# Kernel optimization log

Measured on AMD Instinct MI355X. Metric: run time of the kernel, lower is better.

The kernel has to match this reference:

```python
import jax, jax.numpy as jnp
import numpy as np
from jax import lax

LOOKBACK = 48
HORIZON = 12
INPUT_DIM = 8
OUTPUT_DIM = 1
HIDDEN = 128
NUM_LAYERS = 2
BG_IDX = 0
BATCH = 8192


def _lstm_cell(x, h, c, W_ih, W_hh, b_ih, b_hh):
    # x:[B,Din] h,c:[B,H]; PyTorch gate order i,f,g,o
    g = x @ W_ih.T + h @ W_hh.T + b_ih + b_hh
    i, f, gg, o = jnp.split(g, 4, axis=-1)
    c_new = jax.nn.sigmoid(f) * c + jax.nn.sigmoid(i) * jnp.tanh(gg)
    h_new = jax.nn.sigmoid(o) * jnp.tanh(c_new)
    return h_new, c_new


def setup_inputs() -> dict:
    key = jax.random.key(0)
    ks = jax.random.split(key, 16)
    k_scale = 1.0 / np.sqrt(HIDDEN)
    u = lambda k, shp: jax.random.uniform(k, shp, jnp.float32, -k_scale, k_scale)
    inp = {
        "inputs": jax.random.normal(ks[0], (BATCH, LOOKBACK + HORIZON, INPUT_DIM), jnp.float32),
        "W_ih_0": u(ks[1], (4 * HIDDEN, INPUT_DIM)),
        "W_hh_0": u(ks[2], (4 * HIDDEN, HIDDEN)),
        "b_ih_0": u(ks[3], (4 * HIDDEN,)),
        "b_hh_0": u(ks[4], (4 * HIDDEN,)),
        "W_ih_1": u(ks[5], (4 * HIDDEN, HIDDEN)),
        "W_hh_1": u(ks[6], (4 * HIDDEN, HIDDEN)),
        "b_ih_1": u(ks[7], (4 * HIDDEN,)),
        "b_hh_1": u(ks[8], (4 * HIDDEN,)),
        "W_fc": u(ks[9], (OUTPUT_DIM, HIDDEN)),
        "b_fc": u(ks[10], (OUTPUT_DIM,)),
    }
    return inp


def _forward(inputs, params, W_fc, b_fc):
    B = inputs.shape[0]
    # ---- encode lookback window, layer by layer (time-major scan) ----
    xs = jnp.swapaxes(inputs[:, :LOOKBACK, :], 0, 1)  # [T,B,D]
    finals_h, finals_c = [], []
    for (Wi, Wh, bi, bh) in params:
        h0 = jnp.zeros((B, HIDDEN), inputs.dtype)
        c0 = jnp.zeros((B, HIDDEN), inputs.dtype)
        def cell(carry, x, Wi=Wi, Wh=Wh, bi=bi, bh=bh):
            h, c = carry
            h, c = _lstm_cell(x, h, c, Wi, Wh, bi, bh)
            return (h, c), h
        (hT, cT), xs = lax.scan(cell, (h0, c0), xs)
        finals_h.append(hT)
        finals_c.append(cT)
    hs0 = jnp.stack(finals_h)  # [L,B,H]
    cs0 = jnp.stack(finals_c)

    dec_xs = jnp.swapaxes(inputs[:, LOOKBACK:, :], 0, 1)  # [Th,B,D]
    ts = jnp.arange(HORIZON)

    def step(carry, inp):
        hs, cs, last_bg = carry
        x, t = inp
        bg = jnp.where(t > 0, last_bg, x[:, BG_IDX])
        x = x.at[:, BG_IDX].set(bg)
        new_hs, new_cs = [], []
        cur = x
        for l, (Wi, Wh, bi, bh) in enumerate(params):
            h, c = _lstm_cell(cur, hs[l], cs[l], Wi, Wh, bi, bh)
            new_hs.append(h)
            new_cs.append(c)
            cur = h
        pred = cur @ W_fc.T + b_fc  # [B,O]
        return (jnp.stack(new_hs), jnp.stack(new_cs), pred[:, 0]), pred

    init = (hs0, cs0, jnp.zeros((B,), inputs.dtype))
    _, preds = lax.scan(step, init, (dec_xs, ts))  # [Th,B,O]
    return jnp.swapaxes(preds, 0, 1)  # [B,Th,O]


def reference(inputs, W_ih_0, W_hh_0, b_ih_0, b_hh_0, W_ih_1, W_hh_1, b_ih_1, b_hh_1, W_fc, b_fc):
    params = [(W_ih_0, W_hh_0, b_ih_0, b_hh_0), (W_ih_1, W_hh_1, b_ih_1, b_hh_1)]
    return _forward(inputs, params, W_fc, b_fc)
```

## Files before the change

### kernel.cpp

```cpp
#include <hip/hip_runtime.h>

#define LOOKBACK 48
#define HORIZON  12
#define TTOT     60
#define INPUT_DIM 8
#define HIDDEN   128
#define GATES    512
#define BATCH    8192
#define TILE_B   32
#define NTHREADS 512
#define NSLICES  8
#define L0_KS    5
#define L1_KS    8
#define FRAGS_PER_KS 4
#define FRAG_SHORTS 512
#define KSTRIDE  (FRAGS_PER_KS * FRAG_SHORTS)
#define SLICE_FRAGS ((L0_KS + L1_KS) * FRAGS_PER_KS)
#define W_HALFS  (NSLICES * SLICE_FRAGS * FRAG_SHORTS)

#define ROWP 33
#define A0_CHUNKS 20
#define A1_CHUNKS 16
#define A0_BUF (A0_CHUNKS * ROWP * 8)
#define A1_BUF (A1_CHUNKS * ROWP * 8)
#define A0_HALFS (2 * A0_BUF)
#define A1_HALFS (2 * A1_BUF)

typedef __attribute__((ext_vector_type(8))) _Float16 half8;
typedef __attribute__((ext_vector_type(4))) float f32x4;

__device__ __forceinline__ float frcp(float x) { return __builtin_amdgcn_rcpf(x); }
__device__ __forceinline__ float sigm(float x) {
    return frcp(1.0f + __expf(-x));
}
__device__ __forceinline__ float tanh_fast(float x) {
    float ax = fabsf(x);
    float e  = __expf(-2.0f * ax);
    float t  = (1.0f - e) * frcp(1.0f + e);
    return copysignf(t, x);
}

#define BARRIER() __asm__ volatile("s_waitcnt lgkmcnt(0)\ns_barrier" ::: "memory")

__global__ void setup_kernel(const float* __restrict__ Wih0, const float* __restrict__ Whh0,
                             const float* __restrict__ bi0,  const float* __restrict__ bh0,
                             const float* __restrict__ Wih1, const float* __restrict__ Whh1,
                             const float* __restrict__ bi1,  const float* __restrict__ bh1,
                             _Float16* __restrict__ wfrag, float* __restrict__ bias) {
    int idx = blockIdx.x * blockDim.x + threadIdx.x;
    if (idx < W_HALFS) {
        int e = idx & 511, frag = idx >> 9;
        int lane = e >> 3, j = e & 7;
        int t = frag & 3;
        int rest = frag >> 2;
        int lks = rest % (L0_KS + L1_KS), s = rest / (L0_KS + L1_KS);
        int l = (lks < L0_KS) ? 0 : 1;
        int ks = l ? (lks - L0_KS) : lks;
        int k = ks * 32 + ((lane >> 4) << 3) + j;
        int uu = s * 16 + (lane & 15);
        int row = t * HIDDEN + uu;
        float v = 0.0f;
        if (l == 0) {
            if (k < INPUT_DIM) v = Wih0[row * INPUT_DIM + k];
            else if (k < INPUT_DIM + HIDDEN) v = Whh0[row * HIDDEN + (k - INPUT_DIM)];
        } else {
            if (k < HIDDEN) v = Wih1[row * HIDDEN + k];
            else v = Whh1[row * HIDDEN + (k - HIDDEN)];
        }
        wfrag[idx] = (_Float16)v;
    } else if (idx < W_HALFS + 2 * GATES) {
        int g = idx - W_HALFS;
        bias[g] = (g < GATES) ? (bi0[g] + bh0[g]) : (bi1[g - GATES] + bh1[g - GATES]);
    }
}

__global__ __launch_bounds__(NTHREADS, 2)
void lstm_kernel(const float* __restrict__ input,
                 const _Float16* __restrict__ wfrag,
                 const float* __restrict__ bias01,
                 const float* __restrict__ W_fc,
                 const float* __restrict__ b_fc,
                 float* __restrict__ out) {
    __shared__ _Float16 A0[A0_HALFS];
    __shared__ _Float16 A1[A1_HALFS];
    __shared__ float wfcs[HIDDEN];

    const int tid  = threadIdx.x;
    const int lane = tid & 63;
    const int s    = tid >> 6;
    const int col  = lane & 15;
    const int quad = lane >> 4;
    const int u    = s * 16 + col;
    const int batch0 = blockIdx.x * TILE_B;

    uintptr_t wp64 = (uintptr_t)(wfrag + s * (SLICE_FRAGS * FRAG_SHORTS));
    wp64 = ((uintptr_t)__builtin_amdgcn_readfirstlane((unsigned)(wp64 >> 32)) << 32)
         | __builtin_amdgcn_readfirstlane((unsigned)wp64);
    const _Float16* wbase = (const _Float16*)wp64;

    for (int i = tid; i < A0_HALFS; i += NTHREADS) A0[i] = (_Float16)0.f;
    for (int i = tid; i < A1_HALFS; i += NTHREADS) A1[i] = (_Float16)0.f;
    if (tid < HIDDEN) wfcs[tid] = W_fc[tid];
    const float bfc = b_fc[0];

    float bv0[4], bv1[4];
#pragma unroll
    for (int tt = 0; tt < 4; ++tt) {
        bv0[tt] = bias01[tt * HIDDEN + u];
        bv1[tt] = bias01[GATES + tt * HIDDEN + u];
    }

    float c0[2][4] = {}, c1[2][4] = {};

    float xv = 0.0f;
    if (tid < TILE_B * INPUT_DIM)
        xv = input[(size_t)(batch0 + (tid >> 3)) * (TTOT * INPUT_DIM) + (tid & 7)];
    BARRIER();
    if (tid < TILE_B * INPUT_DIM)
        A0[(tid >> 3) * 8 + (tid & 7)] = (_Float16)xv;

    half8 bq[3][4];
    half8 ah[2][2];

#define LOADB(p, sl) {                                                          \
    _Pragma("unroll") for (int tt = 0; tt < 4; ++tt)                            \
        bq[sl][tt] = *(const half8*)(wbase + (p) * KSTRIDE                      \
                                     + tt * FRAG_SHORTS + lane * 8); }
#define LOADA(H, off, chunk, buf) { int base_ = (off) + ((chunk) * ROWP + col) * 8; \
    ah[buf][0] = *(const half8*)(H + base_);                                    \
    ah[buf][1] = *(const half8*)(H + base_ + 16 * 8); }
#define COMP(ACC, ab, sl)                                                       \
    _Pragma("unroll") for (int tt = 0; tt < 4; ++tt)                            \
    _Pragma("unroll") for (int mt = 0; mt < 2; ++mt)                            \
        ACC[mt][tt] = __builtin_amdgcn_mfma_f32_16x16x32_f16(                   \
            ah[ab][mt], bq[sl][tt], ACC[mt][tt], 0, 0, 0);

    LOADB(0, 0) LOADB(1, 1) LOADB(2, 2)
    BARRIER();

#pragma unroll 1
    for (int t = 0; t < TTOT; ++t) {
        const int rb = t & 1, wb = rb ^ 1;
        const int a0r = rb * A0_BUF, a0w = wb * A0_BUF;
        const int a1r = rb * A1_BUF, a1w = wb * A1_BUF;

        if (tid < TILE_B * INPUT_DIM && t + 1 < TTOT)
            xv = input[(size_t)(batch0 + (tid >> 3)) * (TTOT * INPUT_DIM)
                       + (t + 1) * INPUT_DIM + (tid & 7)];

        f32x4 acc[2][4];
#pragma unroll
        for (int tt = 0; tt < 4; ++tt) {
            f32x4 b = {bv0[tt], bv0[tt], bv0[tt], bv0[tt]};
            acc[0][tt] = b; acc[1][tt] = b;
        }
        LOADA(A0, a0r, quad, 0)
        LOADA(A0, a0r, 4 + quad, 1)  COMP(acc, 0, 0) LOADB(3, 0)
        LOADA(A0, a0r, 8 + quad, 0)  COMP(acc, 1, 1) LOADB(4, 1)
        LOADA(A0, a0r, 12 + quad, 1) COMP(acc, 0, 2) LOADB(5, 2)
        LOADA(A0, a0r, 16 + quad, 0) COMP(acc, 1, 0) LOADB(6, 0)
                                     COMP(acc, 0, 1) LOADB(7, 1)

#pragma unroll
        for (int mt = 0; mt < 2; ++mt) {
#pragma unroll
            for (int r = 0; r < 4; ++r) {
                float ig = sigm(acc[mt][0][r]);
                float fg = sigm(acc[mt][1][r]);
                float gg = tanh_fast(acc[mt][2][r]);
                float og = sigm(acc[mt][3][r]);
                float cn = fg * c0[mt][r] + ig * gg;
                c0[mt][r] = cn;
                float h = og * tanh_fast(cn);
                int row = mt * 16 + quad * 4 + r;
                A0[a0w + ((1 + (u >> 3)) * ROWP + row) * 8 + (u & 7)] = (_Float16)h;
            }
        }
        if (tid < TILE_B * INPUT_DIM && t + 1 < TTOT) {
            int r = tid >> 3, k = tid & 7;
            if (!(t + 1 > LOOKBACK && k == 0))
                A0[a0w + r * 8 + k] = (_Float16)xv;
        }
        BARRIER();

#pragma unroll
        for (int tt = 0; tt < 4; ++tt) {
            f32x4 b = {bv1[tt], bv1[tt], bv1[tt], bv1[tt]};
            acc[0][tt] = b; acc[1][tt] = b;
        }
        LOADA(A0, a0w, 1 + quad, 0)
        LOADA(A0, a0w, 5 + quad, 1)   COMP(acc, 0, 2) LOADB(8, 2)
        LOADA(A0, a0w, 9 + quad, 0)   COMP(acc, 1, 0) LOADB(9, 0)
        LOADA(A0, a0w, 13 + quad, 1)  COMP(acc, 0, 1) LOADB(10, 1)
        LOADA(A1, a1r, quad, 0)       COMP(acc, 1, 2) LOADB(11, 2)
        LOADA(A1, a1r, 4 + quad, 1)   COMP(acc, 0, 0) LOADB(12, 0)
        LOADA(A1, a1r, 8 + quad, 0)   COMP(acc, 1, 1) LOADB(1, 1)
        LOADA(A1, a1r, 12 + quad, 1)  COMP(acc, 0, 2) LOADB(2, 2)
                                      COMP(acc, 1, 0) LOADB(0, 0)

#pragma unroll
        for (int mt = 0; mt < 2; ++mt) {
#pragma unroll
            for (int r = 0; r < 4; ++r) {
                float ig = sigm(acc[mt][0][r]);
                float fg = sigm(acc[mt][1][r]);
                float gg = tanh_fast(acc[mt][2][r]);
                float og = sigm(acc[mt][3][r]);
                float cn = fg * c1[mt][r] + ig * gg;
                c1[mt][r] = cn;
                float h = og * tanh_fast(cn);
                int row = mt * 16 + quad * 4 + r;
                A1[a1w + ((u >> 3) * ROWP + row) * 8 + (u & 7)] = (_Float16)h;
            }
        }

        if (t >= LOOKBACK) {
            BARRIER();
            int r = tid >> 4, sub = tid & 15;
            float p = 0.0f;
#pragma unroll
            for (int i = 0; i < HIDDEN / 16; ++i) {
                int uu = sub + i * 16;
                p += (float)A1[a1w + ((uu >> 3) * ROWP + r) * 8 + (uu & 7)] * wfcs[uu];
            }
#pragma unroll
            for (int off = 8; off; off >>= 1) p += __shfl_down(p, off, 16);
            if (sub == 0) {
                float pr = p + bfc;
                out[(size_t)(batch0 + r) * HORIZON + (t - LOOKBACK)] = pr;
                if (t + 1 < TTOT)
                    A0[a0w + r * 8] = (_Float16)pr;
            }
            BARRIER();
        }
    }
#undef LOADB
#undef LOADA
#undef COMP
}

extern "C" void kernel_launch(void* const* d_in, const int* in_sizes, int n_in,
                              void* d_out, int out_size, void* d_ws, size_t ws_size,
                              hipStream_t stream) {
    const float* input = (const float*)d_in[0];
    const float* Wih0  = (const float*)d_in[1];
    const float* Whh0  = (const float*)d_in[2];
    const float* bi0   = (const float*)d_in[3];
    const float* bh0   = (const float*)d_in[4];
    const float* Wih1  = (const float*)d_in[5];
    const float* Whh1  = (const float*)d_in[6];
    const float* bi1   = (const float*)d_in[7];
    const float* bh1   = (const float*)d_in[8];
    const float* W_fc  = (const float*)d_in[9];
    const float* b_fc  = (const float*)d_in[10];

    _Float16* wfrag = (_Float16*)d_ws;
    float* bias = (float*)((char*)d_ws + (size_t)W_HALFS * sizeof(_Float16));

    int total = W_HALFS + 2 * GATES;
    setup_kernel<<<(total + 255) / 256, 256, 0, stream>>>(
        Wih0, Whh0, bi0, bh0, Wih1, Whh1, bi1, bh1, wfrag, bias);

    lstm_kernel<<<BATCH / TILE_B, NTHREADS, 0, stream>>>(
        input, wfrag, bias, W_fc, b_fc, (float*)d_out);
}
```

Before: 374.5 us.

## Unroll time loop by two and prefetch next step's layer-0 A fragments

The time loop is unrolled by two through a STEP macro, so the double-buffer offsets become compile-time constants. During the lookback phase, the first layer-0 A fragments for the next step are loaded at the end of the current step, so they overlap the tail work instead of stalling the next step's first MFMAs. Decode steps still reload at the start because the fed-back prediction changes the input. tanh is rewritten as 2*sigmoid(2x)-1, which needs fewer instructions but loses some precision near zero and raises register pressure.

Result: no change. 370.9 us (-1.0%).

```diff
diff --git a/kernel.cpp b/kernel.cpp
--- a/kernel.cpp
+++ b/kernel.cpp
@@ -12,10 +12,11 @@
 #define NSLICES  8
 #define L0_KS    5
 #define L1_KS    8
+#define NPOS     (L0_KS + L1_KS)
 #define FRAGS_PER_KS 4
 #define FRAG_SHORTS 512
 #define KSTRIDE  (FRAGS_PER_KS * FRAG_SHORTS)
-#define SLICE_FRAGS ((L0_KS + L1_KS) * FRAGS_PER_KS)
+#define SLICE_FRAGS (NPOS * FRAGS_PER_KS)
 #define W_HALFS  (NSLICES * SLICE_FRAGS * FRAG_SHORTS)
 
 #define ROWP 33
@@ -34,10 +35,7 @@
     return frcp(1.0f + __expf(-x));
 }
 __device__ __forceinline__ float tanh_fast(float x) {
-    float ax = fabsf(x);
-    float e  = __expf(-2.0f * ax);
-    float t  = (1.0f - e) * frcp(1.0f + e);
-    return copysignf(t, x);
+    return __builtin_fmaf(2.0f, frcp(1.0f + __expf(-2.0f * x)), -1.0f);
 }
 
 #define BARRIER() __asm__ volatile("s_waitcnt lgkmcnt(0)\ns_barrier" ::: "memory")
@@ -53,7 +51,7 @@
         int lane = e >> 3, j = e & 7;
         int t = frag & 3;
         int rest = frag >> 2;
-        int lks = rest % (L0_KS + L1_KS), s = rest / (L0_KS + L1_KS);
+        int lks = rest % NPOS, s = rest / NPOS;
         int l = (lks < L0_KS) ? 0 : 1;
         int ks = l ? (lks - L0_KS) : lks;
         int k = ks * 32 + ((lane >> 4) << 3) + j;
@@ -112,12 +110,14 @@
 
     float c0[2][4] = {}, c1[2][4] = {};
 
-    float xv = 0.0f;
-    if (tid < TILE_B * INPUT_DIM)
-        xv = input[(size_t)(batch0 + (tid >> 3)) * (TTOT * INPUT_DIM) + (tid & 7)];
-    BARRIER();
-    if (tid < TILE_B * INPUT_DIM)
-        A0[(tid >> 3) * 8 + (tid & 7)] = (_Float16)xv;
+    {
+        float x0 = 0.0f;
+        if (tid < TILE_B * INPUT_DIM)
+            x0 = input[(size_t)(batch0 + (tid >> 3)) * (TTOT * INPUT_DIM) + (tid & 7)];
+        BARRIER();
+        if (tid < TILE_B * INPUT_DIM)
+            A0[(tid >> 3) * 8 + (tid & 7)] = (_Float16)x0;
+    }
 
     half8 bq[3][4];
     half8 ah[2][2];
@@ -129,7 +129,7 @@
 #define LOADA(H, off, chunk, buf) { int base_ = (off) + ((chunk) * ROWP + col) * 8; \
     ah[buf][0] = *(const half8*)(H + base_);                                    \
     ah[buf][1] = *(const half8*)(H + base_ + 16 * 8); }
-#define COMP(ACC, ab, sl)                                                       \
+#define COMPQ(ACC, ab, sl)                                                      \
     _Pragma("unroll") for (int tt = 0; tt < 4; ++tt)                            \
     _Pragma("unroll") for (int mt = 0; mt < 2; ++mt)                            \
         ACC[mt][tt] = __builtin_amdgcn_mfma_f32_16x16x32_f16(                   \
@@ -137,106 +137,117 @@
 
     LOADB(0, 0) LOADB(1, 1) LOADB(2, 2)
     BARRIER();
+    LOADA(A0, 0, quad, 0)
+    LOADA(A0, 0, 4 + quad, 1)
+
+#define STEP(TC, RB) {                                                          \
+    const int a0r = (RB) * A0_BUF, a0w = ((RB) ^ 1) * A0_BUF;                   \
+    const int a1r = (RB) * A1_BUF, a1w = ((RB) ^ 1) * A1_BUF;                   \
+    float xv = 0.0f;                                                            \
+    if (tid < TILE_B * INPUT_DIM && (TC) + 1 < TTOT)                            \
+        xv = input[(size_t)(batch0 + (tid >> 3)) * (TTOT * INPUT_DIM)           \
+                   + ((TC) + 1) * INPUT_DIM + (tid & 7)];                       \
+                     \
+    if ((TC) > LOOKBACK) {                                                      \
+        LOADA(A0, a0r, quad, 0)                                                 \
+        LOADA(A0, a0r, 4 + quad, 1)                                             \
+    }                                                                           \
+                         \
+    f32x4 acc[2][4];                                                            \
+    _Pragma("unroll") for (int tt = 0; tt < 4; ++tt) {                          \
+        f32x4 b = {bv0[tt], bv0[tt], bv0[tt], bv0[tt]};                         \
+        acc[0][tt] = b; acc[1][tt] = b;                                         \
+    }                                                                           \
+    COMPQ(acc, 0, 0) LOADB(3, 0) LOADA(A0, a0r, 8 + quad, 0)                    \
+    COMPQ(acc, 1, 1) LOADB(4, 1) LOADA(A0, a0r, 12 + quad, 1)                   \
+    COMPQ(acc, 0, 2) LOADB(5, 2) LOADA(A0, a0r, 16 + quad, 0)                   \
+    COMPQ(acc, 1, 0) LOADB(6, 0)                                                \
+    COMPQ(acc, 0, 1) LOADB(7, 1)                                                \
+                                  \
+    _Pragma("unroll") for (int mt = 0; mt < 2; ++mt) {                          \
+        _Pragma("unroll") for (int r = 0; r < 4; ++r) {                         \
+            float ig = sigm(acc[mt][0][r]);                                     \
+            float fg = sigm(acc[mt][1][r]);                                     \
+            float gg = tanh_fast(acc[mt][2][r]);                                \
+            float og = sigm(acc[mt][3][r]);                                     \
+            float cn = fg * c0[mt][r] + ig * gg;                                \
+            c0[mt][r] = cn;                                                     \
+            float h = og * tanh_fast(cn);                                       \
+            int row = mt * 16 + quad * 4 + r;                                   \
+            A0[a0w + ((1 + (u >> 3)) * ROWP + row) * 8 + (u & 7)] = (_Float16)h;\
+        }                                                                       \
+    }                                                                           \
+              \
+    if (tid < TILE_B * INPUT_DIM && (TC) + 1 < TTOT) {                          \
+        int r = tid >> 3, k = tid & 7;                                          \
+        if (!((TC) + 1 > LOOKBACK && k == 0))                                   \
+            A0[a0w + r * 8 + k] = (_Float16)xv;                                 \
+    }                                                                           \
+    BARRIER();                                    \
+       \
+    _Pragma("unroll") for (int tt = 0; tt < 4; ++tt) {                          \
+        f32x4 b = {bv1[tt], bv1[tt], bv1[tt], bv1[tt]};                         \
+        acc[0][tt] = b; acc[1][tt] = b;                                         \
+    }                                                                           \
+    LOADA(A0, a0w, 1 + quad, 0)                                                 \
+    LOADA(A0, a0w, 5 + quad, 1)   COMPQ(acc, 0, 2) LOADB(8, 2)                  \
+    LOADA(A0, a0w, 9 + quad, 0)   COMPQ(acc, 1, 0) LOADB(9, 0)                  \
+    LOADA(A0, a0w, 13 + quad, 1)  COMPQ(acc, 0, 1) LOADB(10, 1)                 \
+    LOADA(A1, a1r, quad, 0)       COMPQ(acc, 1, 2) LOADB(11, 2)                 \
+    LOADA(A1, a1r, 4 + quad, 1)   COMPQ(acc, 0, 0) LOADB(12, 0)                 \
+    LOADA(A1, a1r, 8 + quad, 0)   COMPQ(acc, 1, 1) LOADB(1, 1)                  \
+    LOADA(A1, a1r, 12 + quad, 1)  COMPQ(acc, 0, 2) LOADB(2, 2)                  \
+                                  COMPQ(acc, 1, 0) LOADB(0, 0)                  \
+                                               \
+    _Pragma("unroll") for (int mt = 0; mt < 2; ++mt) {                          \
+        _Pragma("unroll") for (int r = 0; r < 4; ++r) {                         \
+            float ig = sigm(acc[mt][0][r]);                                     \
+            float fg = sigm(acc[mt][1][r]);                                     \
+            float gg = tanh_fast(acc[mt][2][r]);                                \
+            float og = sigm(acc[mt][3][r]);                                     \
+            float cn = fg * c1[mt][r] + ig * gg;                                \
+            c1[mt][r] = cn;                                                     \
+            float h = og * tanh_fast(cn);                                       \
+            int row = mt * 16 + quad * 4 + r;                                   \
+            A1[a1w + ((u >> 3) * ROWP + row) * 8 + (u & 7)] = (_Float16)h;      \
+        }                                                                       \
+    }                                                                           \
+       \
+    if ((TC) < LOOKBACK) {                                                      \
+        LOADA(A0, a0w, quad, 0)                                                 \
+        LOADA(A0, a0w, 4 + quad, 1)                                             \
+    }                                                                           \
+                                     \
+    if ((TC) >= LOOKBACK) {                                                     \
+        BARRIER();                                       \
+        int r = tid >> 4, sub = tid & 15;                                       \
+        float p = 0.0f;                                                         \
+        _Pragma("unroll") for (int i = 0; i < HIDDEN / 16; ++i) {               \
+            int uu = sub + i * 16;                                              \
+            p += (float)A1[a1w + ((uu >> 3) * ROWP + r) * 8 + (uu & 7)]         \
+                 * wfcs[uu];                                                    \
+        }                                                                       \
+        _Pragma("unroll") for (int off = 8; off; off >>= 1)                     \
+            p += __shfl_down(p, off, 16);                                       \
+        if (sub == 0) {                                                         \
+            float pr = p + bfc;                                                 \
+            out[(size_t)(batch0 + r) * HORIZON + ((TC) - LOOKBACK)] = pr;       \
+            if ((TC) + 1 < TTOT)                                                \
+                A0[a0w + r * 8] = (_Float16)pr;                                 \
+        }                                                                       \
+        BARRIER();                                     \
+    }                                                                           \
+}
 
 #pragma unroll 1
-    for (int t = 0; t < TTOT; ++t) {
-        const int rb = t & 1, wb = rb ^ 1;
-        const int a0r = rb * A0_BUF, a0w = wb * A0_BUF;
-        const int a1r = rb * A1_BUF, a1w = wb * A1_BUF;
-
-        if (tid < TILE_B * INPUT_DIM && t + 1 < TTOT)
-            xv = input[(size_t)(batch0 + (tid >> 3)) * (TTOT * INPUT_DIM)
-                       + (t + 1) * INPUT_DIM + (tid & 7)];
-
-        f32x4 acc[2][4];
-#pragma unroll
-        for (int tt = 0; tt < 4; ++tt) {
-            f32x4 b = {bv0[tt], bv0[tt], bv0[tt], bv0[tt]};
-            acc[0][tt] = b; acc[1][tt] = b;
-        }
-        LOADA(A0, a0r, quad, 0)
-        LOADA(A0, a0r, 4 + quad, 1)  COMP(acc, 0, 0) LOADB(3, 0)
-        LOADA(A0, a0r, 8 + quad, 0)  COMP(acc, 1, 1) LOADB(4, 1)
-        LOADA(A0, a0r, 12 + quad, 1) COMP(acc, 0, 2) LOADB(5, 2)
-        LOADA(A0, a0r, 16 + quad, 0) COMP(acc, 1, 0) LOADB(6, 0)
-                                     COMP(acc, 0, 1) LOADB(7, 1)
-
-#pragma unroll
-        for (int mt = 0; mt < 2; ++mt) {
-#pragma unroll
-            for (int r = 0; r < 4; ++r) {
-                float ig = sigm(acc[mt][0][r]);
-                float fg = sigm(acc[mt][1][r]);
-                float gg = tanh_fast(acc[mt][2][r]);
-                float og = sigm(acc[mt][3][r]);
-                float cn = fg * c0[mt][r] + ig * gg;
-                c0[mt][r] = cn;
-                float h = og * tanh_fast(cn);
-                int row = mt * 16 + quad * 4 + r;
-                A0[a0w + ((1 + (u >> 3)) * ROWP + row) * 8 + (u & 7)] = (_Float16)h;
-            }
-        }
-        if (tid < TILE_B * INPUT_DIM && t + 1 < TTOT) {
-            int r = tid >> 3, k = tid & 7;
-            if (!(t + 1 > LOOKBACK && k == 0))
-                A0[a0w + r * 8 + k] = (_Float16)xv;
-        }
-        BARRIER();
-
-#pragma unroll
-        for (int tt = 0; tt < 4; ++tt) {
-            f32x4 b = {bv1[tt], bv1[tt], bv1[tt], bv1[tt]};
-            acc[0][tt] = b; acc[1][tt] = b;
-        }
-        LOADA(A0, a0w, 1 + quad, 0)
-        LOADA(A0, a0w, 5 + quad, 1)   COMP(acc, 0, 2) LOADB(8, 2)
-        LOADA(A0, a0w, 9 + quad, 0)   COMP(acc, 1, 0) LOADB(9, 0)
-        LOADA(A0, a0w, 13 + quad, 1)  COMP(acc, 0, 1) LOADB(10, 1)
-        LOADA(A1, a1r, quad, 0)       COMP(acc, 1, 2) LOADB(11, 2)
-        LOADA(A1, a1r, 4 + quad, 1)   COMP(acc, 0, 0) LOADB(12, 0)
-        LOADA(A1, a1r, 8 + quad, 0)   COMP(acc, 1, 1) LOADB(1, 1)
-        LOADA(A1, a1r, 12 + quad, 1)  COMP(acc, 0, 2) LOADB(2, 2)
-                                      COMP(acc, 1, 0) LOADB(0, 0)
-
-#pragma unroll
-        for (int mt = 0; mt < 2; ++mt) {
-#pragma unroll
-            for (int r = 0; r < 4; ++r) {
-                float ig = sigm(acc[mt][0][r]);
-                float fg = sigm(acc[mt][1][r]);
-                float gg = tanh_fast(acc[mt][2][r]);
-                float og = sigm(acc[mt][3][r]);
-                float cn = fg * c1[mt][r] + ig * gg;
-                c1[mt][r] = cn;
-                float h = og * tanh_fast(cn);
-                int row = mt * 16 + quad * 4 + r;
-                A1[a1w + ((u >> 3) * ROWP + row) * 8 + (u & 7)] = (_Float16)h;
-            }
-        }
-
-        if (t >= LOOKBACK) {
-            BARRIER();
-            int r = tid >> 4, sub = tid & 15;
-            float p = 0.0f;
-#pragma unroll
-            for (int i = 0; i < HIDDEN / 16; ++i) {
-                int uu = sub + i * 16;
-                p += (float)A1[a1w + ((uu >> 3) * ROWP + r) * 8 + (uu & 7)] * wfcs[uu];
-            }
-#pragma unroll
-            for (int off = 8; off; off >>= 1) p += __shfl_down(p, off, 16);
-            if (sub == 0) {
-                float pr = p + bfc;
-                out[(size_t)(batch0 + r) * HORIZON + (t - LOOKBACK)] = pr;
-                if (t + 1 < TTOT)
-                    A0[a0w + r * 8] = (_Float16)pr;
-            }
-            BARRIER();
-        }
-    }
+    for (int t = 0; t < TTOT; t += 2) {
+        STEP(t, 0)
+        STEP(t + 1, 1)
+    }
+#undef STEP
 #undef LOADB
 #undef LOADA
-#undef COMP
+#undef COMPQ
 }
 
 extern "C" void kernel_launch(void* const* d_in, const int* in_sizes, int n_in,
```
